# Kernel tuning notes

Measured on AMD Instinct MI355X. Metric: run time of the kernel, lower is better.

The kernel has to match this reference:

```python
import jax, jax.numpy as jnp
import numpy as np
from jax import lax

E, H, V, S, T, B = 128, 254, 32000, 50, 50, 64


def setup_inputs() -> dict:
    key = jax.random.key(0)
    ks = jax.random.split(key, 14)
    sc = 0.05
    n = lambda k, shape: jax.random.normal(k, shape, dtype=jnp.float32) * sc
    return {
        "src": jax.random.randint(ks[0], (S, B), 0, V),
        "trg": jax.random.randint(ks[1], (T, B), 0, V),
        "emb_enc": n(ks[2], (V, E)),
        "W_ih_e": n(ks[3], (3 * H, E)),
        "W_hh_e": n(ks[4], (3 * H, H)),
        "b_ih_e": n(ks[5], (3 * H,)),
        "b_hh_e": n(ks[6], (3 * H,)),
        "emb_dec": n(ks[7], (V, E)),
        "W_ih_d": n(ks[8], (3 * H, E + H)),
        "W_hh_d": n(ks[9], (3 * H, H)),
        "b_ih_d": n(ks[10], (3 * H,)),
        "b_hh_d": n(ks[11], (3 * H,)),
        "W_out": n(ks[12], (V, E + 2 * H)),
        "b_out": n(ks[13], (V,)),
    }


def _gru_cell(x, h, W_ih, W_hh, b_ih, b_hh):
    # PyTorch GRU cell: gates ordered [r, z, n]
    gi = x @ W_ih.T + b_ih            # [B, 3H]
    gh = h @ W_hh.T + b_hh            # [B, 3H]
    i_r, i_z, i_n = jnp.split(gi, 3, axis=-1)
    h_r, h_z, h_n = jnp.split(gh, 3, axis=-1)
    r = jax.nn.sigmoid(i_r + h_r)
    z = jax.nn.sigmoid(i_z + h_z)
    n = jnp.tanh(i_n + r * h_n)
    return (1.0 - z) * n + z * h


def reference(src, trg, emb_enc, W_ih_e, W_hh_e, b_ih_e, b_hh_e,
              emb_dec, W_ih_d, W_hh_d, b_ih_d, b_hh_d, W_out, b_out):
    dt = emb_enc.dtype
    # --- Encoder: GRU over src (dropout = identity in eval) ---
    enc_emb = emb_enc[src]                       # [S, B, E]
    h0 = jnp.zeros((B, H), dtype=dt)

    def enc_step(h, x):
        h2 = _gru_cell(x, h, W_ih_e, W_hh_e, b_ih_e, b_hh_e)
        return h2, None

    context, _ = lax.scan(enc_step, h0, enc_emb)  # [B, H]

    # --- Decoder: teacher forcing (ratio=1.0) => scan over trg[:-1] ---
    dec_emb = emb_dec[trg[:-1]]                  # [T-1, B, E]

    def dec_step(h, e):
        xc = jnp.concatenate([e, context], axis=-1)          # [B, E+H]
        h2 = _gru_cell(xc, h, W_ih_d, W_hh_d, b_ih_d, b_hh_d)
        feat = jnp.concatenate([h2, context, e], axis=-1)    # [B, E+2H]
        pred = feat @ W_out.T + b_out                        # [B, V]
        return h2, pred

    _, preds = lax.scan(dec_step, context, dec_emb)  # [T-1, B, V]
    outputs = jnp.concatenate(
        [jnp.zeros((1, B, V), dtype=preds.dtype), preds], axis=0)  # [T, B, V]
    return outputs
```

## Files before the change

kernel.cpp:

```cpp
#include <hip/hip_runtime.h>
#include <cstdint>
#include <cstddef>

typedef unsigned short u16;
typedef unsigned int u32;
typedef __attribute__((ext_vector_type(8))) short bf16x8;
typedef __attribute__((ext_vector_type(4))) float f32x4;

#define AS1 __attribute__((address_space(1)))
#define AS3 __attribute__((address_space(3)))

__device__ __forceinline__ float bf2f(u16 u){ u32 x = ((u32)u)<<16; float f; __builtin_memcpy(&f,&x,4); return f; }
__device__ __forceinline__ u16 f2bf(float f){ u32 x; __builtin_memcpy(&x,&f,4); u32 r=(x+0x7FFFu+((x>>16)&1u))>>16; return (u16)r; }

__device__ __forceinline__ float fast_sig(float x){
  return __fdividef(1.f, 1.f + __expf(-x));
}
__device__ __forceinline__ float fast_tanh(float x){
  float e = __expf(2.f*x);
  return 1.f - __fdividef(2.f, e + 1.f);
}

__device__ __forceinline__ void dev_store_u16(u16* p, u16 v){
  __hip_atomic_store(p, v, __ATOMIC_RELAXED, __HIP_MEMORY_SCOPE_AGENT);
}
__device__ __forceinline__ void dev_store_u32(u32* p, u32 v){
  __hip_atomic_store(p, v, __ATOMIC_RELAXED, __HIP_MEMORY_SCOPE_AGENT);
}


__global__ void zero_bytes(uint4* p, size_t n16){
  size_t i = (size_t)blockIdx.x*blockDim.x + threadIdx.x;
  size_t st = (size_t)gridDim.x*blockDim.x;
  uint4 z; z.x=0u; z.y=0u; z.z=0u; z.w=0u;
  for (; i<n16; i+=st) p[i]=z;
}

__global__ void pad_convert_g(const float* __restrict__ src, int src_ld, int c0, int vcols,
                              u16* __restrict__ dst, int dcols){
  int i = blockIdx.x*256 + threadIdx.x;
  int tot = 768*dcols;
  if (i >= tot) return;
  int p = i/dcols, c = i - p*dcols;
  int wv = p/96, rem = p - wv*96, sec = rem>>5, u = rem&31;
  int j = wv*32 + u;
  float v = 0.f;
  if (j < 254 && c < vcols) v = src[(size_t)(sec*254 + j)*src_ld + c0 + c];
  dst[i] = f2bf(v);
}

__global__ void pad_bias_comb(const float* __restrict__ ih, const float* __restrict__ hh,
                              float* __restrict__ dst){
  int p = blockIdx.x*256 + threadIdx.x;
  if (p >= 768) return;
  int wv = p/96, rem = p - wv*96, sec = rem>>5, u = rem&31;
  int j = wv*32 + u;
  float v = 0.f;
  if (j < 254){ v = ih[sec*254 + j]; if (sec < 2) v += hh[sec*254 + j]; }
  dst[p] = v;
}

__global__ void pad_bias_g(const float* __restrict__ src, float* __restrict__ dst){
  int p = blockIdx.x*256 + threadIdx.x;
  if (p >= 768) return;
  int wv = p/96, rem = p - wv*96, sec = rem>>5, u = rem&31;
  int j = wv*32 + u;
  dst[p] = (j<254) ? src[sec*254 + j] : 0.f;
}

__global__ void gather_enc(const int* __restrict__ idx, const float* __restrict__ emb, u16* __restrict__ dst){
  int i = blockIdx.x*256 + threadIdx.x;
  int r = i>>7, k = i&127;
  dst[i] = f2bf(emb[(size_t)idx[r]*128 + k]);
}

__global__ void gather_dec(const int* __restrict__ idx, const float* __restrict__ emb,
                           u16* __restrict__ dst, u16* __restrict__ feat){
  int i = blockIdx.x*256 + threadIdx.x;
  int r = i>>7, k = i&127;
  u16 v = 0;
  if (r < 3136) v = f2bf(emb[(size_t)idx[r]*128 + k]);
  dst[i] = v;
  if (r < 3136) feat[(size_t)r*640 + 508 + k] = v;
}


__global__ __launch_bounds__(256) void gemm_bt(
  const u16* __restrict__ A, int lda,
  const u16* __restrict__ B, int ldb,
  float* __restrict__ C, long long ldc,
  const float* __restrict__ bias,
  int K, int Mtiles, int Mstore)
{
  __shared__ __align__(16) u16 Abuf[2][128*64];
  __shared__ __align__(16) u16 Bbuf[2][128*64];
  const int t = threadIdx.x;
  const int w = t>>6, l = t&63;
  const int wm = w>>1, wn = w&1;
  const int mt = blockIdx.x % Mtiles, nt = blockIdx.x / Mtiles;
  const int m0 = mt<<7, n0 = nt<<7;

  const int lr = l>>3, lg = l&7;

  auto stage = [&](const u16* __restrict__ G, int ld, int base0, int k0, u16* Lbuf){
    #pragma unroll
    for (int i=0;i<4;++i){
      const int rbase = i*32 + w*8;
      const int r = rbase + lr;
      const int gsw = lg ^ (r&7);
      __builtin_amdgcn_global_load_lds(
        (const AS1 void*)(G + (size_t)(base0+r)*ld + k0 + gsw*8),
        (AS3 void*)(Lbuf + rbase*64), 16, 0, 0);
    }
  };

  f32x4 acc[4][4] = {};
  const int ksteps = K>>6;

  stage(A, lda, m0, 0, Abuf[0]);
  stage(B, ldb, n0, 0, Bbuf[0]);
  asm volatile("s_waitcnt vmcnt(0)" ::: "memory");
  __syncthreads();

  for (int ks=0; ks<ksteps; ++ks){
    const int cb = ks&1;
    if (ks+1 < ksteps){
      stage(A, lda, m0, (ks+1)<<6, Abuf[cb^1]);
      stage(B, ldb, n0, (ks+1)<<6, Bbuf[cb^1]);
    }
    const u16* Al = Abuf[cb];
    const u16* Bl = Bbuf[cb];
    #pragma unroll
    for (int kk=0;kk<2;++kk){
      const int ko = kk*32 + (l>>4)*8;
      bf16x8 af[4], bfr[4];
      #pragma unroll
      for (int m=0;m<4;++m){
        const int row = wm*64+m*16+(l&15);
        af[m] = *(const bf16x8*)&Al[row*64 + (ko ^ ((row&7)<<3))];
      }
      #pragma unroll
      for (int n=0;n<4;++n){
        const int row = wn*64+n*16+(l&15);
        bfr[n] = *(const bf16x8*)&Bl[row*64 + (ko ^ ((row&7)<<3))];
      }
      #pragma unroll
      for (int m=0;m<4;++m)
        #pragma unroll
        for (int n=0;n<4;++n)
          acc[m][n] = __builtin_amdgcn_mfma_f32_16x16x32_bf16(af[m], bfr[n], acc[m][n], 0,0,0);
    }
    asm volatile("s_waitcnt vmcnt(0)" ::: "memory");
    __syncthreads();
  }

  float bv[4];
  #pragma unroll
  for (int n=0;n<4;++n) bv[n] = bias[n0 + wn*64 + n*16 + (l&15)];
  #pragma unroll
  for (int m=0;m<4;++m){
    const int rb = m0 + wm*64 + m*16 + (l>>4)*4;
    #pragma unroll
    for (int n=0;n<4;++n){
      const int col = n0 + wn*64 + n*16 + (l&15);
      #pragma unroll
      for (int r=0;r<4;++r){
        const int rr = rb + r;
        if (rr < Mstore) C[(size_t)rr*ldc + col] = acc[m][n][r] + bv[n];
      }
    }
  }
}


__global__ __launch_bounds__(512,1) void fused_scan_gemm(
  const u16* Whhe, const u16* Whhd, const u16* Wihdc,
  const float* bhhe, const float* bhhd,
  const float* enc_gi, const float* dec_gi,
  u16* feat, u16* wout_b, const float* W_out,
  float* Cg, const float* b_out, u32* ctr)
{
  __shared__ __align__(16) char smem[139776];
  const int t = threadIdx.x;
  const int w = t>>6, l = t&63;

  if (blockIdx.x < 4){
    const int g = blockIdx.x;
    const int la = l&15, q = l>>4;
    const int brow0 = g*16;

    u16*   hb   = (u16*)smem;
    float* gib  = (float*)(smem + 16896);
    u16*   ctxb = (u16*)(smem + 115200);

    bf16x8 Bf[48];

    auto loadW = [&](const u16* __restrict__ W){
      #pragma unroll
      for (int nt=0; nt<6; ++nt)
        #pragma unroll
        for (int kk=0; kk<8; ++kk)
          Bf[nt*8+kk] = *(const bf16x8*)&W[(size_t)(w*96 + nt*16 + la)*256 + kk*32 + q*8];
    };

    auto stage = [&](const float* __restrict__ gsrc, int step, float* dstL){
      const float* src = gsrc + (size_t)(step*64 + brow0)*768;
      #pragma unroll
      for (int i=0;i<6;++i){
        const int base = i*2048 + w*256;
        __builtin_amdgcn_global_load_lds((const AS1 void*)(src + base + l*4),
                                         (AS3 void*)(dstL + base), 16, 0, 0);
      }
    };

    auto mm = [&](const u16* hsrc, f32x4* acc){
      #pragma unroll
      for (int kk=0; kk<8; ++kk){
        bf16x8 a = *(const bf16x8*)&hsrc[la*264 + kk*32 + q*8];
        #pragma unroll
        for (int nt=0; nt<6; ++nt)
          acc[nt] = __builtin_amdgcn_mfma_f32_16x16x32_bf16(a, Bf[nt*8+kk], acc[nt], 0,0,0);
      }
    };

    for (int i=t; i<2*16*264; i+=512) hb[i] = 0;
    stage(enc_gi, 0, gib);
    loadW(Whhe);
    float bn[2];
    #pragma unroll
    for (int tl=0; tl<2; ++tl) bn[tl] = bhhe[w*96 + tl*16 + la + 64];
    asm volatile("s_waitcnt vmcnt(0)" ::: "memory");
    __syncthreads();

    #pragma unroll 1
    for (int s=0; s<50; ++s){
      const int cur = s&1;
      if (s < 49) stage(enc_gi, s+1, gib + (cur^1)*12288);
      f32x4 acc[6] = {};
      mm(hb + cur*4224, acc);
      #pragma unroll
      for (int tl=0; tl<2; ++tl){
        const int pb = w*96 + tl*16 + la;
        const int j  = w*32 + tl*16 + la;
        #pragma unroll
        for (int r=0;r<4;++r){
          const int b = q*4 + r;
          const float gir = gib[cur*12288 + b*768 + pb];
          const float giz = gib[cur*12288 + b*768 + pb + 32];
          const float gin = gib[cur*12288 + b*768 + pb + 64];
          const float ho = bf2f(hb[cur*4224 + b*264 + j]);
          const float rg = fast_sig(gir + acc[tl][r]);
          const float zg = fast_sig(giz + acc[2+tl][r]);
          const float ng = fast_tanh(gin + rg*(acc[4+tl][r] + bn[tl]));
          hb[(cur^1)*4224 + b*264 + j] = f2bf((1.f-zg)*ng + zg*ho);
        }
      }
      asm volatile("s_waitcnt vmcnt(0)" ::: "memory");
      __syncthreads();
    }

    stage(dec_gi, 0, gib);

    loadW(Wihdc);
    {
      f32x4 acc[6] = {};
      mm(hb, acc);
      #pragma unroll
      for (int nt=0; nt<6; ++nt)
        #pragma unroll
        for (int r=0;r<4;++r)
          ctxb[(q*4+r)*768 + w*96 + nt*16 + la] = f2bf(acc[nt][r]);
    }

    #pragma unroll 1
    for (int i=t; i<49*4096; i+=512){
      const int tt = i>>12, rem = i&4095, b = rem>>8, c = rem&255;
      if (c < 254) dev_store_u16(&feat[(size_t)(tt*64 + brow0 + b)*640 + 254 + c], hb[b*264 + c]);
    }

    loadW(Whhd);
    #pragma unroll
    for (int tl=0; tl<2; ++tl) bn[tl] = bhhd[w*96 + tl*16 + la + 64];
    asm volatile("s_waitcnt vmcnt(0)" ::: "memory");
    __syncthreads();

    #pragma unroll 1
    for (int tt=0; tt<49; ++tt){
      const int cur = tt&1;
      if (tt < 48) stage(dec_gi, tt+1, gib + (cur^1)*12288);
      f32x4 acc[6] = {};
      mm(hb + cur*4224, acc);
      #pragma unroll
      for (int tl=0; tl<2; ++tl){
        const int pb = w*96 + tl*16 + la;
        const int j  = w*32 + tl*16 + la;
        #pragma unroll
        for (int r=0;r<4;++r){
          const int b = q*4 + r;
          const float gir = gib[cur*12288 + b*768 + pb]      + bf2f(ctxb[b*768 + pb]);
          const float giz = gib[cur*12288 + b*768 + pb + 32] + bf2f(ctxb[b*768 + pb + 32]);
          const float gin = gib[cur*12288 + b*768 + pb + 64] + bf2f(ctxb[b*768 + pb + 64]);
          const float ho = bf2f(hb[cur*4224 + b*264 + j]);
          const float rg = fast_sig(gir + acc[tl][r]);
          const float zg = fast_sig(giz + acc[2+tl][r]);
          const float ng = fast_tanh(gin + rg*(acc[4+tl][r] + bn[tl]));
          const float h2 = (1.f-zg)*ng + zg*ho;
          const u16 hbv = f2bf(h2);
          hb[(cur^1)*4224 + b*264 + j] = hbv;
          if (j < 254) dev_store_u16(&feat[(size_t)(tt*64 + brow0 + b)*640 + j], hbv);
        }
      }
      asm volatile("s_waitcnt vmcnt(0)" ::: "memory");
      __syncthreads();
      if (t==0) dev_store_u32(&ctr[g], (u32)(tt+1));
    }
    return;
  }

  const int bg = blockIdx.x - 4;
  const int wm = w>>2, wn = w&3;
  const int la = l&15, q = l>>4;
  const int lr = l>>3, lg = l&7;

  u16* AL = (u16*)smem;
  u16* BL = (u16*)(smem + 32768);

  if (bg < 125){
    const int n0c = bg<<8;
    #pragma unroll 1
    for (int i=t; i<256*80; i+=512){
      const int r = i/80, c8 = (i - r*80)<<3;
      u16 o[8];
      #pragma unroll
      for (int jj=0;jj<8;++jj){
        const int c = c8 + jj;
        o[jj] = (c < 636) ? f2bf(W_out[(size_t)(n0c+r)*636 + c]) : (u16)0;
      }
      u32* dst = (u32*)&wout_b[(size_t)(n0c+r)*640 + c8];
      const u32* sv = (const u32*)o;
      #pragma unroll
      for (int jj=0;jj<4;++jj) dev_store_u32(&dst[jj], sv[jj]);
    }
    asm volatile("s_waitcnt vmcnt(0)" ::: "memory");
    __syncthreads();
    if (t==0) dev_store_u32(&ctr[32 + bg], 1u);
  }

  const int nsleep = 1 + (bg&3);
  #pragma unroll 1
  for (int tau = bg; tau < 3125; tau += 248){
    const int mt = tau/125, nt = tau - mt*125;
    const int m0 = mt<<7, n0 = nt<<8;
    const u32 need = (u32)((2*mt+2 < 49) ? (2*mt+2) : 49);

    if (w==0){
      int cnt = 0;
      while (true){
        u32 v  = (l<4) ? __hip_atomic_load(&ctr[l], __ATOMIC_RELAXED, __HIP_MEMORY_SCOPE_AGENT) : 0xFFFFFFFFu;
        u32 wf = (l==4) ? __hip_atomic_load(&ctr[32 + nt], __ATOMIC_RELAXED, __HIP_MEMORY_SCOPE_AGENT) : 1u;
        if (__all((int)((v >= need) && (wf != 0u)))) break;
        for (int z=0; z<nsleep; ++z) __builtin_amdgcn_s_sleep(16);
        if (++cnt > (1<<22)) break;
      }
    }
    __syncthreads();

    auto stageA = [&](int k0, int buf){
      #pragma unroll
      for (int i=0;i<2;++i){
        const int rbase = i*64 + w*8;
        const int r = rbase + lr;
        __builtin_amdgcn_global_load_lds(
          (const AS1 void*)(feat + (size_t)(m0+r)*640 + k0 + ((lg^lr)<<3)),
          (AS3 void*)(AL + buf*8192 + rbase*64), 16, 0, 0);
      }
    };
    auto stageB = [&](int k0, int buf){
      #pragma unroll
      for (int i=0;i<4;++i){
        const int rbase = i*64 + w*8;
        const int r = rbase + lr;
        __builtin_amdgcn_global_load_lds(
          (const AS1 void*)(wout_b + (size_t)(n0+r)*640 + k0 + ((lg^lr)<<3)),
          (AS3 void*)(BL + buf*16384 + rbase*64), 16, 0, 0);
      }
    };

    f32x4 acc[4][4] = {};
    stageA(0,0); stageB(0,0);
    asm volatile("s_waitcnt vmcnt(0)" ::: "memory");
    __syncthreads();

    #pragma unroll 1
    for (int ks=0; ks<10; ++ks){
      const int cb = ks&1;
      if (ks < 9){ stageA((ks+1)<<6, cb^1); stageB((ks+1)<<6, cb^1); }
      const u16* Alp = AL + cb*8192;
      const u16* Blp = BL + cb*16384;
      #pragma unroll
      for (int kk=0;kk<2;++kk){
        const int ko = kk*32 + q*8;
        bf16x8 af[4], bfr[4];
        #pragma unroll
        for (int m=0;m<4;++m){
          const int row = wm*64 + m*16 + la;
          af[m] = *(const bf16x8*)&Alp[row*64 + (ko ^ ((row&7)<<3))];
        }
        #pragma unroll
        for (int n=0;n<4;++n){
          const int row = wn*64 + n*16 + la;
          bfr[n] = *(const bf16x8*)&Blp[row*64 + (ko ^ ((row&7)<<3))];
        }
        #pragma unroll
        for (int m=0;m<4;++m)
          #pragma unroll
          for (int n=0;n<4;++n)
            acc[m][n] = __builtin_amdgcn_mfma_f32_16x16x32_bf16(af[m], bfr[n], acc[m][n], 0,0,0);
      }
      asm volatile("s_waitcnt vmcnt(0)" ::: "memory");
      __syncthreads();
    }

    float bv[4];
    #pragma unroll
    for (int n=0;n<4;++n) bv[n] = b_out[n0 + wn*64 + n*16 + la];
    #pragma unroll
    for (int m=0;m<4;++m){
      const int rb = m0 + wm*64 + m*16 + q*4;
      #pragma unroll
      for (int n=0;n<4;++n){
        const int col = n0 + wn*64 + n*16 + la;
        #pragma unroll
        for (int r=0;r<4;++r){
          const int rr = rb + r;
          if (rr < 3136)
            __builtin_nontemporal_store(acc[m][n][r] + bv[n], &Cg[(size_t)rr*32000 + col]);
        }
      }
    }
  }
}


extern "C" void kernel_launch(void* const* d_in, const int* in_sizes, int n_in,
                              void* d_out, int out_size, void* d_ws, size_t ws_size,
                              hipStream_t stream) {
  const int*   src     = (const int*)d_in[0];
  const int*   trg     = (const int*)d_in[1];
  const float* emb_enc = (const float*)d_in[2];
  const float* W_ih_e  = (const float*)d_in[3];
  const float* W_hh_e  = (const float*)d_in[4];
  const float* b_ih_e  = (const float*)d_in[5];
  const float* b_hh_e  = (const float*)d_in[6];
  const float* emb_dec = (const float*)d_in[7];
  const float* W_ih_d  = (const float*)d_in[8];
  const float* W_hh_d  = (const float*)d_in[9];
  const float* b_ih_d  = (const float*)d_in[10];
  const float* b_hh_d  = (const float*)d_in[11];
  const float* W_out   = (const float*)d_in[12];
  const float* b_out   = (const float*)d_in[13];
  float* out = (float*)d_out;

  char* basep = (char*)d_ws;
  size_t off = 0;
  auto take = [&](size_t b)->char*{ char* p = basep + off; off = (off + b + 255) & ~(size_t)255; return p; };
  u16* feat    = (u16*)take(4096000);
  u32* ctr     = (u32*)take(4096);
  u16* wout_b  = (u16*)take(40960000);
  u16* wihe_b  = (u16*)take(196608);
  u16* wihde_b = (u16*)take(196608);
  u16* wihdc_b = (u16*)take(393216);
  u16* whhe_b  = (u16*)take(393216);
  u16* whhd_b  = (u16*)take(393216);
  u16* encx_b  = (u16*)take(819200);
  u16* dece_b  = (u16*)take(819200);
  float* enc_gi = (float*)take(9830400);
  float* dec_gi = (float*)take(9830400);
  float* bihe_p = (float*)take(3072);
  float* bihd_p = (float*)take(3072);
  float* bhhe_p = (float*)take(3072);
  float* bhhd_p = (float*)take(3072);
  (void)in_sizes; (void)n_in; (void)out_size; (void)ws_size;

  zero_bytes<<<1, 256, 0, stream>>>((uint4*)ctr, (size_t)(4096/16));
  zero_bytes<<<2000, 256, 0, stream>>>((uint4*)out, (size_t)(8192000/16));

  pad_convert_g<<<384, 256, 0, stream>>>(W_ih_e, 128,   0, 128, wihe_b, 128);
  pad_convert_g<<<384, 256, 0, stream>>>(W_ih_d, 382,   0, 128, wihde_b, 128);
  pad_convert_g<<<768, 256, 0, stream>>>(W_ih_d, 382, 128, 254, wihdc_b, 256);
  pad_convert_g<<<768, 256, 0, stream>>>(W_hh_e, 254,   0, 254, whhe_b, 256);
  pad_convert_g<<<768, 256, 0, stream>>>(W_hh_d, 254,   0, 254, whhd_b, 256);

  pad_bias_comb<<<3, 256, 0, stream>>>(b_ih_e, b_hh_e, bihe_p);
  pad_bias_comb<<<3, 256, 0, stream>>>(b_ih_d, b_hh_d, bihd_p);
  pad_bias_g<<<3, 256, 0, stream>>>(b_hh_e, bhhe_p);
  pad_bias_g<<<3, 256, 0, stream>>>(b_hh_d, bhhd_p);

  gather_enc<<<1600, 256, 0, stream>>>(src, emb_enc, encx_b);
  gather_dec<<<1600, 256, 0, stream>>>(trg, emb_dec, dece_b, feat);

  gemm_bt<<<25*6, 256, 0, stream>>>(encx_b, 128, wihe_b, 128, enc_gi, (long long)768, bihe_p, 128, 25, 3200);
  gemm_bt<<<25*6, 256, 0, stream>>>(dece_b, 128, wihde_b, 128, dec_gi, (long long)768, bihd_p, 128, 25, 3200);

  fused_scan_gemm<<<252, 512, 0, stream>>>(whhe_b, whhd_b, wihdc_b, bhhe_p, bhhd_p,
                                           enc_gi, dec_gi, feat, wout_b, W_out,
                                           out + (size_t)64*32000, b_out, ctr);
}
```

Before: 560.1 us.

## Store input-gate preactivations in bf16 and triple-buffer GRU scan prefetch

The input-projection GEMMs now write bf16 instead of fp32, which halves the gate-preactivation traffic and the LDS staging buffer. The recurrent scan prefetches two steps ahead with a three-slot ring and uses partial vmcnt waits in place of full drains, so per-step feat stores no longer block the barrier. The progress counter is published one step later, and the context copy into feat uses 32-bit stores. This risks bf16 rounding error in the gate inputs and depends on correct hand-tuned vmcnt counts for ordering.

```diff
diff --git a/kernel.cpp b/kernel.cpp
--- a/kernel.cpp
+++ b/kernel.cpp
@@ -85,10 +85,10 @@
 }
 
 
-__global__ __launch_bounds__(256) void gemm_bt(
+__global__ __launch_bounds__(256) void gemm_bt16(
   const u16* __restrict__ A, int lda,
   const u16* __restrict__ B, int ldb,
-  float* __restrict__ C, long long ldc,
+  u16* __restrict__ C, long long ldc,
   const float* __restrict__ bias,
   int K, int Mtiles, int Mstore)
 {
@@ -166,7 +166,7 @@
       #pragma unroll
       for (int r=0;r<4;++r){
         const int rr = rb + r;
-        if (rr < Mstore) C[(size_t)rr*ldc + col] = acc[m][n][r] + bv[n];
+        if (rr < Mstore) C[(size_t)rr*ldc + col] = f2bf(acc[m][n][r] + bv[n]);
       }
     }
   }
@@ -176,11 +176,11 @@
 __global__ __launch_bounds__(512,1) void fused_scan_gemm(
   const u16* Whhe, const u16* Whhd, const u16* Wihdc,
   const float* bhhe, const float* bhhd,
-  const float* enc_gi, const float* dec_gi,
+  const u16* enc_gi, const u16* dec_gi,
   u16* feat, u16* wout_b, const float* W_out,
   float* Cg, const float* b_out, u32* ctr)
 {
-  __shared__ __align__(16) char smem[139776];
+  __shared__ __align__(16) char smem[115200];
   const int t = threadIdx.x;
   const int w = t>>6, l = t&63;
 
@@ -189,9 +189,9 @@
     const int la = l&15, q = l>>4;
     const int brow0 = g*16;
 
-    u16*   hb   = (u16*)smem;
-    float* gib  = (float*)(smem + 16896);
-    u16*   ctxb = (u16*)(smem + 115200);
+    u16* hb   = (u16*)smem;
+    u16* gib  = (u16*)(smem + 16896);
+    u16* ctxb = (u16*)(smem + 90624);
 
     bf16x8 Bf[48];
 
@@ -203,13 +203,13 @@
           Bf[nt*8+kk] = *(const bf16x8*)&W[(size_t)(w*96 + nt*16 + la)*256 + kk*32 + q*8];
     };
 
-    auto stage = [&](const float* __restrict__ gsrc, int step, float* dstL){
-      const float* src = gsrc + (size_t)(step*64 + brow0)*768;
-      #pragma unroll
-      for (int i=0;i<6;++i){
-        const int base = i*2048 + w*256;
-        __builtin_amdgcn_global_load_lds((const AS1 void*)(src + base + l*4),
-                                         (AS3 void*)(dstL + base), 16, 0, 0);
+    auto stage = [&](const u16* __restrict__ gsrc, int step, u16* dstL){
+      const u16* src = gsrc + (size_t)(step*64 + brow0)*768;
+      #pragma unroll
+      for (int i=0;i<3;++i){
+        const int off = i*4096 + w*512;
+        __builtin_amdgcn_global_load_lds((const AS1 void*)(src + off + l*8),
+                                         (AS3 void*)(dstL + off), 16, 0, 0);
       }
     };
 
@@ -224,20 +224,22 @@
     };
 
     for (int i=t; i<2*16*264; i+=512) hb[i] = 0;
-    stage(enc_gi, 0, gib);
     loadW(Whhe);
     float bn[2];
     #pragma unroll
     for (int tl=0; tl<2; ++tl) bn[tl] = bhhe[w*96 + tl*16 + la + 64];
-    asm volatile("s_waitcnt vmcnt(0)" ::: "memory");
-    __syncthreads();
+    stage(enc_gi, 0, gib);
+    stage(enc_gi, 1, gib + 12288);
+    asm volatile("s_waitcnt vmcnt(0) lgkmcnt(0)" ::: "memory");
+    __builtin_amdgcn_s_barrier();
 
     #pragma unroll 1
     for (int s=0; s<50; ++s){
-      const int cur = s&1;
-      if (s < 49) stage(enc_gi, s+1, gib + (cur^1)*12288);
+      const int hc = s&1;
+      const u16* gcur = gib + (s%3)*12288;
+      if (s+2 < 50) stage(enc_gi, s+2, gib + ((s+2)%3)*12288);
       f32x4 acc[6] = {};
-      mm(hb + cur*4224, acc);
+      mm(hb + hc*4224, acc);
       #pragma unroll
       for (int tl=0; tl<2; ++tl){
         const int pb = w*96 + tl*16 + la;
@@ -245,21 +247,23 @@
         #pragma unroll
         for (int r=0;r<4;++r){
           const int b = q*4 + r;
-          const float gir = gib[cur*12288 + b*768 + pb];
-          const float giz = gib[cur*12288 + b*768 + pb + 32];
-          const float gin = gib[cur*12288 + b*768 + pb + 64];
-          const float ho = bf2f(hb[cur*4224 + b*264 + j]);
+          const float gir = bf2f(gcur[b*768 + pb]);
+          const float giz = bf2f(gcur[b*768 + pb + 32]);
+          const float gin = bf2f(gcur[b*768 + pb + 64]);
+          const float ho = bf2f(hb[hc*4224 + b*264 + j]);
           const float rg = fast_sig(gir + acc[tl][r]);
           const float zg = fast_sig(giz + acc[2+tl][r]);
           const float ng = fast_tanh(gin + rg*(acc[4+tl][r] + bn[tl]));
-          hb[(cur^1)*4224 + b*264 + j] = f2bf((1.f-zg)*ng + zg*ho);
+          hb[(hc^1)*4224 + b*264 + j] = f2bf((1.f-zg)*ng + zg*ho);
         }
       }
-      asm volatile("s_waitcnt vmcnt(0)" ::: "memory");
-      __syncthreads();
+      if (s+2 < 50) asm volatile("s_waitcnt vmcnt(3) lgkmcnt(0)" ::: "memory");
+      else          asm volatile("s_waitcnt vmcnt(0) lgkmcnt(0)" ::: "memory");
+      __builtin_amdgcn_s_barrier();
     }
 
     stage(dec_gi, 0, gib);
+    stage(dec_gi, 1, gib + 12288);
 
     loadW(Wihdc);
     {
@@ -273,23 +277,27 @@
     }
 
     #pragma unroll 1
-    for (int i=t; i<49*4096; i+=512){
-      const int tt = i>>12, rem = i&4095, b = rem>>8, c = rem&255;
-      if (c < 254) dev_store_u16(&feat[(size_t)(tt*64 + brow0 + b)*640 + 254 + c], hb[b*264 + c]);
+    for (int i=t; i<49*2048; i+=512){
+      const int tt = i>>11, rem = i&2047, b = rem>>7, c2 = rem&127;
+      if (c2 < 127){
+        u32 v = *(const u32*)&hb[b*264 + c2*2];
+        dev_store_u32((u32*)&feat[(size_t)(tt*64 + brow0 + b)*640 + 254 + c2*2], v);
+      }
     }
 
     loadW(Whhd);
     #pragma unroll
     for (int tl=0; tl<2; ++tl) bn[tl] = bhhd[w*96 + tl*16 + la + 64];
-    asm volatile("s_waitcnt vmcnt(0)" ::: "memory");
-    __syncthreads();
+    asm volatile("s_waitcnt vmcnt(0) lgkmcnt(0)" ::: "memory");
+    __builtin_amdgcn_s_barrier();
 
     #pragma unroll 1
     for (int tt=0; tt<49; ++tt){
-      const int cur = tt&1;
-      if (tt < 48) stage(dec_gi, tt+1, gib + (cur^1)*12288);
+      const int hc = tt&1;
+      const u16* gcur = gib + (tt%3)*12288;
+      if (tt+2 < 49) stage(dec_gi, tt+2, gib + ((tt+2)%3)*12288);
       f32x4 acc[6] = {};
-      mm(hb + cur*4224, acc);
+      mm(hb + hc*4224, acc);
       #pragma unroll
       for (int tl=0; tl<2; ++tl){
         const int pb = w*96 + tl*16 + la;
@@ -297,23 +305,27 @@
         #pragma unroll
         for (int r=0;r<4;++r){
           const int b = q*4 + r;
-          const float gir = gib[cur*12288 + b*768 + pb]      + bf2f(ctxb[b*768 + pb]);
-          const float giz = gib[cur*12288 + b*768 + pb + 32] + bf2f(ctxb[b*768 + pb + 32]);
-          const float gin = gib[cur*12288 + b*768 + pb + 64] + bf2f(ctxb[b*768 + pb + 64]);
-          const float ho = bf2f(hb[cur*4224 + b*264 + j]);
+          const float gir = bf2f(gcur[b*768 + pb])      + bf2f(ctxb[b*768 + pb]);
+          const float giz = bf2f(gcur[b*768 + pb + 32]) + bf2f(ctxb[b*768 + pb + 32]);
+          const float gin = bf2f(gcur[b*768 + pb + 64]) + bf2f(ctxb[b*768 + pb + 64]);
+          const float ho = bf2f(hb[hc*4224 + b*264 + j]);
           const float rg = fast_sig(gir + acc[tl][r]);
           const float zg = fast_sig(giz + acc[2+tl][r]);
           const float ng = fast_tanh(gin + rg*(acc[4+tl][r] + bn[tl]));
           const float h2 = (1.f-zg)*ng + zg*ho;
           const u16 hbv = f2bf(h2);
-          hb[(cur^1)*4224 + b*264 + j] = hbv;
+          hb[(hc^1)*4224 + b*264 + j] = hbv;
           if (j < 254) dev_store_u16(&feat[(size_t)(tt*64 + brow0 + b)*640 + j], hbv);
         }
       }
-      asm volatile("s_waitcnt vmcnt(0)" ::: "memory");
-      __syncthreads();
-      if (t==0) dev_store_u32(&ctr[g], (u32)(tt+1));
-    }
+      if (tt+2 < 49) asm volatile("s_waitcnt vmcnt(11) lgkmcnt(0)" ::: "memory");
+      else           asm volatile("s_waitcnt vmcnt(8) lgkmcnt(0)"  ::: "memory");
+      __builtin_amdgcn_s_barrier();
+      if (t==0) dev_store_u32(&ctr[g], (u32)tt);
+    }
+    asm volatile("s_waitcnt vmcnt(0)" ::: "memory");
+    __syncthreads();
+    if (t==0) dev_store_u32(&ctr[g], 49u);
     return;
   }
 
@@ -474,8 +486,8 @@
   u16* whhd_b  = (u16*)take(393216);
   u16* encx_b  = (u16*)take(819200);
   u16* dece_b  = (u16*)take(819200);
-  float* enc_gi = (float*)take(9830400);
-  float* dec_gi = (float*)take(9830400);
+  u16* enc_gi  = (u16*)take(4915200);
+  u16* dec_gi  = (u16*)take(4915200);
   float* bihe_p = (float*)take(3072);
   float* bihd_p = (float*)take(3072);
   float* bhhe_p = (float*)take(3072);
@@ -499,8 +511,8 @@
   gather_enc<<<1600, 256, 0, stream>>>(src, emb_enc, encx_b);
   gather_dec<<<1600, 256, 0, stream>>>(trg, emb_dec, dece_b, feat);
 
-  gemm_bt<<<25*6, 256, 0, stream>>>(encx_b, 128, wihe_b, 128, enc_gi, (long long)768, bihe_p, 128, 25, 3200);
-  gemm_bt<<<25*6, 256, 0, stream>>>(dece_b, 128, wihde_b, 128, dec_gi, (long long)768, bihd_p, 128, 25, 3200);
+  gemm_bt16<<<25*6, 256, 0, stream>>>(encx_b, 128, wihe_b, 128, enc_gi, (long long)768, bihe_p, 128, 25, 3200);
+  gemm_bt16<<<25*6, 256, 0, stream>>>(dece_b, 128, wihde_b, 128, dec_gi, (long long)768, bihd_p, 128, 25, 3200);
 
   fused_scan_gemm<<<252, 512, 0, stream>>>(whhe_b, whhd_b, wihdc_b, bhhe_p, bhhd_p,
                                            enc_gi, dec_gi, feat, wout_b, W_out,
```

Result: faster. 518.3 us (-7.5%).
